# Performance work log

Hardware: AMD Instinct MI355X
Metric: run time of the kernel (lower is better)

Reference implementation:

```python
import math
import jax, jax.numpy as jnp
import numpy as np

B, S, D, H, DK, DV, L, DFF, V, NC, HID = 16, 512, 512, 8, 64, 64, 6, 2048, 32000, 5, 64


def setup_inputs() -> dict:
    key = jax.random.key(0)
    ks = jax.random.split(key, 32)
    def n(k, shape, scale=0.02):
        return jax.random.normal(k, shape, jnp.float32) * scale
    input_ids = jax.random.randint(ks[0], (B, S), 0, V).astype(jnp.int32)
    attention_mask = jnp.ones((B, S), jnp.bool_)
    emb = n(ks[1], (V, D)).at[0].set(0.0)  # padding_idx=0 row zeroed
    cls_token = jnp.zeros((D,), jnp.float32)
    return {
        "input_ids": input_ids,
        "attention_mask": attention_mask,
        "emb": emb,
        "cls_token": cls_token,
        "ln1_g": jnp.ones((L, D), jnp.float32), "ln1_b": jnp.zeros((L, D), jnp.float32),
        "ln2_g": jnp.ones((L, D), jnp.float32), "ln2_b": jnp.zeros((L, D), jnp.float32),
        "Wq": n(ks[2], (L, H, D, DK)), "bq": n(ks[3], (L, H, DK)),
        "Wk": n(ks[4], (L, H, D, DK)), "bk": n(ks[5], (L, H, DK)),
        "Wv": n(ks[6], (L, H, D, DV)), "bv": n(ks[7], (L, H, DV)),
        "Wo": n(ks[8], (L, H * DV, D)), "bo": n(ks[9], (L, D)),
        "W1": n(ks[10], (L, D, DFF)), "b1": n(ks[11], (L, DFF)),
        "W2": n(ks[12], (L, DFF, D)), "b2": n(ks[13], (L, D)),
        "Wc1": n(ks[14], (D, HID)), "bc1": n(ks[15], (HID,)),
        "Wc2": n(ks[16], (HID, NC)), "bc2": n(ks[17], (NC,)),
    }


def _layernorm(x, g, b, eps=1e-5):
    mu = jnp.mean(x, axis=-1, keepdims=True)
    var = jnp.var(x, axis=-1, keepdims=True)
    return (x - mu) * jax.lax.rsqrt(var + eps) * g + b


def _sinusoidal_pe(seq_len, d_model):
    pos = jnp.arange(seq_len, dtype=jnp.float32)[:, None]
    div = jnp.exp(jnp.arange(0, d_model, 2, dtype=jnp.float32) * (-math.log(10000.0) / d_model))
    pe = jnp.zeros((seq_len, d_model), jnp.float32)
    pe = pe.at[:, 0::2].set(jnp.sin(pos * div))
    pe = pe.at[:, 1::2].set(jnp.cos(pos * div))
    return pe


def _forward(input_ids, attention_mask, emb, cls_token,
             ln1_g, ln1_b, ln2_g, ln2_b,
             Wq, bq, Wk, bk, Wv, bv, Wo, bo,
             W1, b1, W2, b2, Wc1, bc1, Wc2, bc2):
    b, s = input_ids.shape
    x = emb[input_ids]                                     # [B,S,D]
    cls = jnp.broadcast_to(cls_token[None, None, :], (b, 1, x.shape[-1]))
    x = jnp.concatenate([cls, x], axis=1)                  # [B,S+1,D]
    full_mask = jnp.concatenate([jnp.ones((b, 1), jnp.bool_), attention_mask], axis=1)
    # pairwise attention mask [B, T, T]
    pair_mask = full_mask[:, None, :] & full_mask[:, :, None]
    x = x + _sinusoidal_pe(s + 1, x.shape[-1])[None]

    scale = 1.0 / math.sqrt(DK)

    def block(x, p):
        g1, be1, g2, be2, wq, bq_, wk, bk_, wv, bv_, wo, bo_, w1, bb1, w2, bb2 = p
        h = _layernorm(x, g1, be1)
        q = jnp.einsum('btd,hdk->bhtk', h, wq) + bq_[None, :, None, :]
        k = jnp.einsum('btd,hdk->bhtk', h, wk) + bk_[None, :, None, :]
        v = jnp.einsum('btd,hdv->bhtv', h, wv) + bv_[None, :, None, :]
        scores = jnp.einsum('bhqk,bhtk->bhqt', q, k) * scale
        scores = jnp.where(pair_mask[:, None, :, :], scores, -jnp.inf)
        attn = jax.nn.softmax(scores, axis=-1)
        o = jnp.einsum('bhqt,bhtv->bhqv', attn, v)          # [B,H,T,DV]
        o = o.transpose(0, 2, 1, 3).reshape(x.shape[0], x.shape[1], H * DV)
        x = x + o @ wo + bo_
        h2 = _layernorm(x, g2, be2)
        x = x + jnp.maximum(h2 @ w1 + bb1, 0.0) @ w2 + bb2
        return x, None

    params = (ln1_g, ln1_b, ln2_g, ln2_b, Wq, bq, Wk, bk, Wv, bv, Wo, bo, W1, b1, W2, b2)
    x, _ = jax.lax.scan(block, x, params)
    cls_out = x[:, 0]
    logits = jnp.maximum(cls_out @ Wc1 + bc1, 0.0) @ Wc2 + bc2
    return logits


def reference(input_ids, attention_mask, emb, cls_token,
              ln1_g, ln1_b, ln2_g, ln2_b,
              Wq, bq, Wk, bk, Wv, bv, Wo, bo,
              W1, b1, W2, b2, Wc1, bc1, Wc2, bc2):
    return _forward(input_ids, attention_mask, emb, cls_token,
                    ln1_g, ln1_b, ln2_g, ln2_b,
                    Wq, bq, Wk, bk, Wv, bv, Wo, bo,
                    W1, b1, W2, b2, Wc1, bc1, Wc2, bc2)
```

## Files before the change

kernel.cpp:

```cpp
#include <hip/hip_runtime.h>
#include <math.h>

#define DEV __device__ __forceinline__

typedef __attribute__((ext_vector_type(8))) short short8;
typedef __attribute__((ext_vector_type(4))) float f32x4;

DEV unsigned short f2bf(float f) {
  union { float f; unsigned int i; } v; v.f = f;
  unsigned int r = v.i + 0x7fffu + ((v.i >> 16) & 1u);
  return (unsigned short)(r >> 16);
}

DEV void lds16(const void* g, void* l) {
  __builtin_amdgcn_global_load_lds((__attribute__((address_space(1))) void*)(g),
                                   (__attribute__((address_space(3))) void*)(l), 16, 0, 0);
}


__global__ void transpose_g(const float* __restrict__ src, unsigned short* __restrict__ dst,
                            int Ksz, int Nsz) {
  __shared__ float tile[32][33];
  const int tx = threadIdx.x, ty = threadIdx.y;
  const int n0 = blockIdx.x * 32, k0 = blockIdx.y * 32;
  const size_t base = (size_t)blockIdx.z * Ksz * Nsz;
#pragma unroll
  for (int i = 0; i < 4; ++i)
    tile[ty + i * 8][tx] = src[base + (size_t)(k0 + ty + i * 8) * Nsz + n0 + tx];
  __syncthreads();
#pragma unroll
  for (int i = 0; i < 4; ++i)
    dst[base + (size_t)(n0 + ty + i * 8) * Ksz + k0 + tx] = f2bf(tile[tx][ty + i * 8]);
}

__global__ void pack_qkvT(const float* __restrict__ Wq, const float* __restrict__ Wk,
                          const float* __restrict__ Wv, unsigned short* __restrict__ dst) {
  __shared__ float tile[32][33];
  const int tx = threadIdx.x, ty = threadIdx.y;
  const int n0 = blockIdx.x * 32, k0 = blockIdx.y * 32, l = blockIdx.z;
  const int mat = n0 >> 9, hh = (n0 >> 6) & 7, dk0 = n0 & 63;
  const float* W = (mat == 0) ? Wq : (mat == 1) ? Wk : Wv;
  const float* Wl = W + ((size_t)l * 8 + hh) * 512 * 64;
#pragma unroll
  for (int i = 0; i < 4; ++i)
    tile[ty + i * 8][tx] = Wl[(size_t)(k0 + ty + i * 8) * 64 + dk0 + tx];
  __syncthreads();
#pragma unroll
  for (int i = 0; i < 4; ++i)
    dst[(size_t)l * 1536 * 512 + (size_t)(n0 + ty + i * 8) * 512 + k0 + tx] =
        f2bf(tile[tx][ty + i * 8]);
}

__global__ void pack_bias(const float* __restrict__ bq, const float* __restrict__ bk,
                          const float* __restrict__ bv, float* __restrict__ dst) {
  int i = blockIdx.x * 256 + threadIdx.x;
  if (i >= 6 * 1536) return;
  int l = i / 1536, c = i % 1536;
  float v = (c < 512) ? bq[l * 512 + c] : (c < 1024) ? bk[l * 512 + (c - 512)]
                                                     : bv[l * 512 + (c - 1024)];
  dst[i] = v;
}

__global__ void embed_kernel(const int* __restrict__ ids, const float* __restrict__ emb,
                             const float* __restrict__ cls, float* __restrict__ x) {
  int idx = blockIdx.x * 256 + threadIdx.x;
  int m = idx >> 9, d = idx & 511;
  int b = m / 513, t = m % 513;
  float v = (t == 0) ? cls[d] : emb[(size_t)ids[b * 512 + (t - 1)] * 512 + d];
  float fr = -(float)(d & ~1) * (9.2103403719761836f / 512.0f);
  float ang = (float)t * expf(fr);
  float pe = (d & 1) ? cosf(ang) : sinf(ang);
  x[idx] = v + pe;
}

template <int FUSE>
__global__ __launch_bounds__(256) void ln_kernel(float* __restrict__ x,
                                                 const float* __restrict__ g,
                                                 const float* __restrict__ bb,
                                                 unsigned short* __restrict__ h,
                                                 const float* __restrict__ part) {
  int wid = threadIdx.x >> 6, lane = threadIdx.x & 63;
  int m = blockIdx.x * 4 + wid;
  float* xr = x + (size_t)m * 512;
  float4 a = *(const float4*)(xr + lane * 8);
  float4 c = *(const float4*)(xr + lane * 8 + 4);
  if constexpr (FUSE) {
    const size_t PN = 8208ull * 512;
    const float* p = part + (size_t)m * 512 + lane * 8;
    float4 q0 = *(const float4*)(p),          q0b = *(const float4*)(p + 4);
    float4 q1 = *(const float4*)(p + PN),     q1b = *(const float4*)(p + PN + 4);
    float4 q2 = *(const float4*)(p + 2 * PN), q2b = *(const float4*)(p + 2 * PN + 4);
    a.x += q0.x + q1.x + q2.x;  a.y += q0.y + q1.y + q2.y;
    a.z += q0.z + q1.z + q2.z;  a.w += q0.w + q1.w + q2.w;
    c.x += q0b.x + q1b.x + q2b.x;  c.y += q0b.y + q1b.y + q2b.y;
    c.z += q0b.z + q1b.z + q2b.z;  c.w += q0b.w + q1b.w + q2b.w;
    *(float4*)(xr + lane * 8) = a;
    *(float4*)(xr + lane * 8 + 4) = c;
  }
  float s = a.x + a.y + a.z + a.w + c.x + c.y + c.z + c.w;
  float q = a.x * a.x + a.y * a.y + a.z * a.z + a.w * a.w +
            c.x * c.x + c.y * c.y + c.z * c.z + c.w * c.w;
#pragma unroll
  for (int d = 1; d < 64; d <<= 1) { s += __shfl_xor(s, d); q += __shfl_xor(q, d); }
  float mu = s * (1.f / 512.f);
  float var = q * (1.f / 512.f) - mu * mu;
  float rs = 1.f / sqrtf(var + 1e-5f);
  float4 g0 = *(const float4*)(g + lane * 8), g1 = *(const float4*)(g + lane * 8 + 4);
  float4 b0 = *(const float4*)(bb + lane * 8), b1 = *(const float4*)(bb + lane * 8 + 4);
  short8 ov;
  ov[0] = (short)f2bf((a.x - mu) * rs * g0.x + b0.x);
  ov[1] = (short)f2bf((a.y - mu) * rs * g0.y + b0.y);
  ov[2] = (short)f2bf((a.z - mu) * rs * g0.z + b0.z);
  ov[3] = (short)f2bf((a.w - mu) * rs * g0.w + b0.w);
  ov[4] = (short)f2bf((c.x - mu) * rs * g1.x + b1.x);
  ov[5] = (short)f2bf((c.y - mu) * rs * g1.y + b1.y);
  ov[6] = (short)f2bf((c.z - mu) * rs * g1.z + b1.z);
  ov[7] = (short)f2bf((c.w - mu) * rs * g1.w + b1.w);
  *(short8*)(h + (size_t)m * 512 + lane * 8) = ov;
}

template <int EPI>
DEV void gemm_epilogue(f32x4 (&acc)[4][4], const float* __restrict__ bias,
                       unsigned short* __restrict__ Cbf, float* __restrict__ Cres,
                       unsigned short* __restrict__ vT, float* __restrict__ part,
                       int M, int N, int m0, int n0, int wm, int wn, int l15, int l4,
                       int bz) {
  const bool z0 = (bz == 0);
  const size_t MN = (size_t)M * N;
#pragma unroll
  for (int i = 0; i < 4; ++i) {
#pragma unroll
    for (int j = 0; j < 4; ++j) {
      const int gn = n0 + wn + j * 16 + l15;
      float bv = bias[gn];
      if constexpr (EPI == 2) {
        if (!z0) bv = 0.f;
      }
#pragma unroll
      for (int r = 0; r < 4; ++r) {
        const int gm = m0 + wm + i * 16 + l4 * 4 + r;
        if (gm < M) {
          float v = acc[i][j][r] + bv;
          if constexpr (EPI == 1) v = fmaxf(v, 0.f);
          if constexpr (EPI == 2) {
            if (z0) {
              Cres[(size_t)gm * N + gn] += v;
            } else {
              part[(size_t)(bz - 1) * MN + (size_t)gm * N + gn] = v;
            }
          } else if constexpr (EPI == 3) {
            if (gn < 1024) {
              Cbf[(size_t)gm * N + gn] = f2bf(v);
            } else {
              int b = gm / 513, t = gm - b * 513;
              vT[(size_t)(b * 512 + (gn - 1024)) * 528 + t] = f2bf(v);
            }
          } else {
            Cbf[(size_t)gm * N + gn] = f2bf(v);
          }
        }
      }
    }
  }
}

template <int EPI>
__global__ __launch_bounds__(256) void gemm_bt(const unsigned short* __restrict__ A,
                                               const unsigned short* __restrict__ Bt,
                                               const float* __restrict__ bias,
                                               unsigned short* __restrict__ Cbf,
                                               float* __restrict__ Cres,
                                               unsigned short* __restrict__ vT,
                                               float* __restrict__ part,
                                               int M, int N, int K, int lda) {
  __shared__ __align__(16) unsigned short As[128 * 64];
  __shared__ __align__(16) unsigned short Bs[128 * 64];
  const int tid = threadIdx.x, w = tid >> 6, lane = tid & 63;
  const int l15 = lane & 15, l4 = lane >> 4;
  const int gx = gridDim.x;
  const int nwg = gx * gridDim.y;
  const int id = blockIdx.y * gx + blockIdx.x;
  const int xcd = id & 7, orig = id >> 3;
  const int qq = nwg >> 3, rr = nwg & 7;
  const int newid = (xcd < rr ? xcd * (qq + 1) : rr * (qq + 1) + (xcd - rr) * qq) + orig;
  const int m0 = (newid % gx) * 128, n0 = (newid / gx) * 128;
  const int wm = (w >> 1) * 64, wn = (w & 1) * 64;
  const int kbase = blockIdx.z * K;
  f32x4 acc[4][4] = {};
  const int nk = K >> 6;
  for (int kt = 0; kt < nk; ++kt) {
#pragma unroll
    for (int r = 0; r < 4; ++r) {
      int ol = (r * 4 + w) * 1024 + lane * 16;
      int ra = ol >> 7, cp = (ol >> 4) & 7;
      int co = ((cp ^ (ra & 7)) * 8) + kt * 64;
      lds16(A + (size_t)(m0 + ra) * lda + kbase + co, (char*)As + (r * 4 + w) * 1024);
      lds16(Bt + (size_t)(n0 + ra) * lda + kbase + co, (char*)Bs + (r * 4 + w) * 1024);
    }
    __syncthreads();
#pragma unroll
    for (int kk = 0; kk < 2; ++kk) {
      short8 af[4], bfr[4];
#pragma unroll
      for (int i = 0; i < 4; ++i) {
        int ar = wm + i * 16 + l15;
        af[i] = *(const short8*)&As[ar * 64 + (((kk * 4 + l4) ^ (ar & 7)) * 8)];
        int br = wn + i * 16 + l15;
        bfr[i] = *(const short8*)&Bs[br * 64 + (((kk * 4 + l4) ^ (br & 7)) * 8)];
      }
#pragma unroll
      for (int i = 0; i < 4; ++i)
#pragma unroll
        for (int j = 0; j < 4; ++j)
          acc[i][j] = __builtin_amdgcn_mfma_f32_16x16x32_bf16(af[i], bfr[j], acc[i][j], 0, 0, 0);
    }
    __syncthreads();
  }
  gemm_epilogue<EPI>(acc, bias, Cbf, Cres, vT, part, M, N, m0, n0, wm, wn, l15, l4,
                     blockIdx.z);
}

template <int EPI>
__global__ __launch_bounds__(512) void gemm_wide(const unsigned short* __restrict__ A,
                                                 const unsigned short* __restrict__ Bt,
                                                 const float* __restrict__ bias,
                                                 unsigned short* __restrict__ Cbf,
                                                 float* __restrict__ Cres,
                                                 unsigned short* __restrict__ vT,
                                                 float* __restrict__ part,
                                                 int M, int N, int K, int lda) {
  __shared__ __align__(16) unsigned short As[128 * 64];
  __shared__ __align__(16) unsigned short Bs[256 * 64];
  const int tid = threadIdx.x, w = tid >> 6, lane = tid & 63;
  const int l15 = lane & 15, l4 = lane >> 4;
  const int gx = gridDim.x;
  const int nwg = gx * gridDim.y;
  const int id = blockIdx.y * gx + blockIdx.x;
  const int xcd = id & 7, orig = id >> 3;
  const int qq = nwg >> 3, rr = nwg & 7;
  const int newid = (xcd < rr ? xcd * (qq + 1) : rr * (qq + 1) + (xcd - rr) * qq) + orig;
  const int m0 = (newid % gx) * 128, n0 = (newid / gx) * 256;
  const int wm = (w >> 2) * 64, wn = (w & 3) * 64;
  const int kbase = blockIdx.z * K;
  f32x4 acc[4][4] = {};
  const int nk = K >> 6;
  for (int kt = 0; kt < nk; ++kt) {
#pragma unroll
    for (int r = 0; r < 2; ++r) {
      int s = r * 8 + w;
      int ol = s * 1024 + lane * 16;
      int ra = ol >> 7, cp = (ol >> 4) & 7;
      int co = ((cp ^ (ra & 7)) * 8) + kt * 64;
      lds16(A + (size_t)(m0 + ra) * lda + kbase + co, (char*)As + s * 1024);
    }
#pragma unroll
    for (int r = 0; r < 4; ++r) {
      int s = r * 8 + w;
      int ol = s * 1024 + lane * 16;
      int rb = ol >> 7, cp = (ol >> 4) & 7;
      int co = ((cp ^ (rb & 7)) * 8) + kt * 64;
      lds16(Bt + (size_t)(n0 + rb) * lda + kbase + co, (char*)Bs + s * 1024);
    }
    __syncthreads();
#pragma unroll
    for (int kk = 0; kk < 2; ++kk) {
      short8 af[4], bfr[4];
#pragma unroll
      for (int i = 0; i < 4; ++i) {
        int ar = wm + i * 16 + l15;
        af[i] = *(const short8*)&As[ar * 64 + (((kk * 4 + l4) ^ (ar & 7)) * 8)];
        int br = wn + i * 16 + l15;
        bfr[i] = *(const short8*)&Bs[br * 64 + (((kk * 4 + l4) ^ (br & 7)) * 8)];
      }
#pragma unroll
      for (int i = 0; i < 4; ++i)
#pragma unroll
        for (int j = 0; j < 4; ++j)
          acc[i][j] = __builtin_amdgcn_mfma_f32_16x16x32_bf16(af[i], bfr[j], acc[i][j], 0, 0, 0);
    }
    __syncthreads();
  }
  gemm_epilogue<EPI>(acc, bias, Cbf, Cres, vT, part, M, N, m0, n0, wm, wn, l15, l4,
                     blockIdx.z);
}

__global__ __launch_bounds__(256) void reduce3(const float* __restrict__ p,
                                               float* __restrict__ x) {
  const size_t PN = 8208ull * 512;
  size_t i = ((size_t)blockIdx.x * 256 + threadIdx.x) * 4;
  float4 a = *(const float4*)(x + i);
  float4 b0 = *(const float4*)(p + i);
  float4 b1 = *(const float4*)(p + PN + i);
  float4 b2 = *(const float4*)(p + 2 * PN + i);
  a.x += b0.x + b1.x + b2.x;
  a.y += b0.y + b1.y + b2.y;
  a.z += b0.z + b1.z + b2.z;
  a.w += b0.w + b1.w + b2.w;
  *(float4*)(x + i) = a;
}

__global__ __launch_bounds__(256) void attn_kernel(const unsigned short* __restrict__ qkv,
                                                   const unsigned short* __restrict__ vT,
                                                   unsigned short* __restrict__ o) {
  const int qt = blockIdx.x, bh = blockIdx.y;
  const int b = bh >> 3, hh = bh & 7;
  const int tid = threadIdx.x, w = tid >> 6, lane = tid & 63;
  const int l15 = lane & 15, l4 = lane >> 4;
  __shared__ __align__(16) unsigned short Ks[64 * 64];
  __shared__ __align__(16) unsigned short Vs[64 * 64];
  __shared__ __align__(16) unsigned short Ps[64 * 72];
  const int q0 = qt * 64;
  const size_t qbase = (size_t)b * 513 * 1536;
  short8 qf[2];
  {
    const unsigned short* qp =
        qkv + qbase + (size_t)(q0 + w * 16 + l15) * 1536 + hh * 64 + l4 * 8;
    qf[0] = *(const short8*)qp;
    qf[1] = *(const short8*)(qp + 32);
  }
  f32x4 oacc[4] = {};
  float lpart[4] = {};
  for (int kvt = 0; kvt < 9; ++kvt) {
    const int kv0 = kvt * 64;
#pragma unroll
    for (int r = 0; r < 2; ++r) {
      int ol = (r * 4 + w) * 1024 + lane * 16;
      int rk = ol >> 7, cp = (ol >> 4) & 7;
      int sw = (cp ^ (rk & 7)) * 8;
      lds16(qkv + qbase + (size_t)(kv0 + rk) * 1536 + 512 + hh * 64 + sw,
            (char*)Ks + ol);
      lds16(vT + (size_t)(bh * 64 + rk) * 528 + kv0 + sw, (char*)Vs + ol);
    }
    __syncthreads();
    f32x4 sacc[4] = {};
#pragma unroll
    for (int kk = 0; kk < 2; ++kk)
#pragma unroll
      for (int nf = 0; nf < 4; ++nf) {
        int kr = nf * 16 + l15;
        short8 kf = *(const short8*)&Ks[kr * 64 + (((kk * 4 + l4) ^ (kr & 7)) * 8)];
        sacc[nf] = __builtin_amdgcn_mfma_f32_16x16x32_bf16(qf[kk], kf, sacc[nf], 0, 0, 0);
      }
#pragma unroll
    for (int nf = 0; nf < 4; ++nf) {
      const bool valid = (kv0 + nf * 16 + l15) < 513;
#pragma unroll
      for (int r = 0; r < 4; ++r) {
        float p = valid ? __expf(sacc[nf][r] * 0.125f) : 0.f;
        lpart[r] += p;
        Ps[(w * 16 + l4 * 4 + r) * 72 + nf * 16 + l15] = f2bf(p);
      }
    }
#pragma unroll
    for (int kk = 0; kk < 2; ++kk) {
      short8 pa = *(const short8*)&Ps[(w * 16 + l15) * 72 + kk * 32 + l4 * 8];
#pragma unroll
      for (int nf = 0; nf < 4; ++nf) {
        int dvr = nf * 16 + l15;
        short8 vf = *(const short8*)&Vs[dvr * 64 + (((kk * 4 + l4) ^ (dvr & 7)) * 8)];
        oacc[nf] = __builtin_amdgcn_mfma_f32_16x16x32_bf16(pa, vf, oacc[nf], 0, 0, 0);
      }
    }
    __syncthreads();
  }
#pragma unroll
  for (int d = 1; d < 16; d <<= 1)
#pragma unroll
    for (int r = 0; r < 4; ++r) lpart[r] += __shfl_xor(lpart[r], d);
#pragma unroll
  for (int nf = 0; nf < 4; ++nf)
#pragma unroll
    for (int r = 0; r < 4; ++r) {
      int q = q0 + w * 16 + l4 * 4 + r;
      if (q < 513) {
        float val = oacc[nf][r] / lpart[r];
        o[((size_t)b * 513 + q) * 512 + hh * 64 + nf * 16 + l15] = f2bf(val);
      }
    }
}

__global__ void cls_kernel(const float* __restrict__ x, const float* __restrict__ Wc1,
                           const float* __restrict__ bc1, const float* __restrict__ Wc2,
                           const float* __restrict__ bc2, float* __restrict__ out) {
  int b = blockIdx.x, j = threadIdx.x;
  const float* xr = x + (size_t)b * 513 * 512;
  float acc = bc1[j];
  for (int d = 0; d < 512; ++d) acc += xr[d] * Wc1[d * 64 + j];
  acc = fmaxf(acc, 0.f);
  __shared__ float hid[64];
  hid[j] = acc;
  __syncthreads();
  if (j < 5) {
    float lg = bc2[j];
#pragma unroll
    for (int d2 = 0; d2 < 64; ++d2) lg += hid[d2] * Wc2[d2 * 5 + j];
    out[b * 5 + j] = lg;
  }
}

extern "C" void kernel_launch(void* const* d_in, const int* in_sizes, int n_in,
                              void* d_out, int out_size, void* d_ws, size_t ws_size,
                              hipStream_t stream) {
  const int* ids = (const int*)d_in[0];
  const float* emb = (const float*)d_in[2];
  const float* cls = (const float*)d_in[3];
  const float* ln1g = (const float*)d_in[4];
  const float* ln1b = (const float*)d_in[5];
  const float* ln2g = (const float*)d_in[6];
  const float* ln2b = (const float*)d_in[7];
  const float* Wq = (const float*)d_in[8];
  const float* bq = (const float*)d_in[9];
  const float* Wk = (const float*)d_in[10];
  const float* bk = (const float*)d_in[11];
  const float* Wv = (const float*)d_in[12];
  const float* bv = (const float*)d_in[13];
  const float* Wo = (const float*)d_in[14];
  const float* bo = (const float*)d_in[15];
  const float* W1 = (const float*)d_in[16];
  const float* b1 = (const float*)d_in[17];
  const float* W2 = (const float*)d_in[18];
  const float* b2 = (const float*)d_in[19];
  const float* Wc1 = (const float*)d_in[20];
  const float* bc1 = (const float*)d_in[21];
  const float* Wc2 = (const float*)d_in[22];
  const float* bc2 = (const float*)d_in[23];

  char* ws = (char*)d_ws;
  size_t off = 0;
  auto alloc = [&](size_t bytes) {
    char* p = ws + off;
    off += (bytes + 255) & ~(size_t)255;
    return p;
  };
  const size_t QKV_ELEMS = 8320ull * 1536;
  const size_t VT_ELEMS = 16ull * 512 * 528 + 528;
  const size_t FFN_ELEMS = 8320ull * 2048;
  const size_t BIGU = (QKV_ELEMS + VT_ELEMS > FFN_ELEMS) ? QKV_ELEMS + VT_ELEMS : FFN_ELEMS;

  unsigned short* wqkvT = (unsigned short*)alloc(6ull * 1536 * 512 * 2);
  unsigned short* woT = (unsigned short*)alloc(6ull * 512 * 512 * 2);
  unsigned short* w1T = (unsigned short*)alloc(6ull * 2048 * 512 * 2);
  unsigned short* w2T = (unsigned short*)alloc(6ull * 512 * 2048 * 2);
  float* bqkv = (float*)alloc(6ull * 1536 * 4);
  float* x = (float*)alloc(8208ull * 512 * 4);
  unsigned short* hbuf = (unsigned short*)alloc(8320ull * 512 * 2);
  unsigned short* obuf = (unsigned short*)alloc(8320ull * 512 * 2);
  unsigned short* big = (unsigned short*)alloc(BIGU * 2);
  float* fpart = (float*)alloc(3ull * 8208 * 512 * 4);
  unsigned short* vT = big + QKV_ELEMS;
  if (off > ws_size) return;

  hipMemsetAsync(hbuf + 8208ull * 512, 0, 112ull * 512 * 2, stream);
  hipMemsetAsync(obuf + 8208ull * 512, 0, 112ull * 512 * 2, stream);
  hipMemsetAsync(big + 8208ull * 1536, 0, 112ull * 1536 * 2, stream);
  hipMemsetAsync(vT, 0, VT_ELEMS * 2, stream);

  pack_qkvT<<<dim3(48, 16, 6), dim3(32, 8), 0, stream>>>(Wq, Wk, Wv, wqkvT);
  transpose_g<<<dim3(16, 16, 6), dim3(32, 8), 0, stream>>>(Wo, woT, 512, 512);
  transpose_g<<<dim3(64, 16, 6), dim3(32, 8), 0, stream>>>(W1, w1T, 512, 2048);
  transpose_g<<<dim3(16, 64, 6), dim3(32, 8), 0, stream>>>(W2, w2T, 2048, 512);
  pack_bias<<<36, 256, 0, stream>>>(bq, bk, bv, bqkv);
  embed_kernel<<<16416, 256, 0, stream>>>(ids, emb, cls, x);

  for (int l = 0; l < 6; ++l) {
    if (l == 0)
      ln_kernel<0><<<2052, 256, 0, stream>>>(x, ln1g + l * 512, ln1b + l * 512, hbuf,
                                             nullptr);
    else
      ln_kernel<1><<<2052, 256, 0, stream>>>(x, ln1g + l * 512, ln1b + l * 512, hbuf,
                                             fpart);
    gemm_wide<3><<<dim3(65, 6), 512, 0, stream>>>(hbuf, wqkvT + (size_t)l * 1536 * 512,
                                                  bqkv + l * 1536, big, nullptr, vT,
                                                  nullptr, 8208, 1536, 512, 512);
    attn_kernel<<<dim3(9, 128), 256, 0, stream>>>(big, vT, obuf);
    gemm_bt<2><<<dim3(65, 4), 256, 0, stream>>>(obuf, woT + (size_t)l * 512 * 512,
                                                bo + l * 512, nullptr, x, nullptr,
                                                nullptr, 8208, 512, 512, 512);
    ln_kernel<0><<<2052, 256, 0, stream>>>(x, ln2g + l * 512, ln2b + l * 512, hbuf,
                                           nullptr);
    gemm_wide<1><<<dim3(65, 8), 512, 0, stream>>>(hbuf, w1T + (size_t)l * 2048 * 512,
                                                  b1 + l * 2048, big, nullptr, nullptr,
                                                  nullptr, 8208, 2048, 512, 512);
    gemm_wide<2><<<dim3(65, 2, 4), 512, 0, stream>>>(big, w2T + (size_t)l * 512 * 2048,
                                                     b2 + l * 512, nullptr, x, nullptr,
                                                     fpart, 8208, 512, 512, 2048);
  }
  reduce3<<<4104, 256, 0, stream>>>(fpart, x);
  cls_kernel<<<16, 64, 0, stream>>>(x, Wc1, bc1, Wc2, bc2, (float*)d_out);
}
```

Before: 1.292 ms.

## Double-buffer LDS tiles in GEMM and attention kernels to overlap loads

Both GEMM kernels and the attention kernel now keep two LDS buffers. Each iteration issues the async global-to-LDS loads for the next K or KV tile before running the MFMA work on the current tile. This removes the barrier that sat between load and compute, so global-load latency can overlap with matrix math. The cost is double the LDS footprint (96KB for gemm_wide), which may cut how many blocks fit on each CU.

```diff
diff --git a/kernel.cpp b/kernel.cpp
--- a/kernel.cpp
+++ b/kernel.cpp
@@ -173,8 +173,8 @@
                                                unsigned short* __restrict__ vT,
                                                float* __restrict__ part,
                                                int M, int N, int K, int lda) {
-  __shared__ __align__(16) unsigned short As[128 * 64];
-  __shared__ __align__(16) unsigned short Bs[128 * 64];
+  __shared__ __align__(16) unsigned short As[2][128 * 64];
+  __shared__ __align__(16) unsigned short Bs[2][128 * 64];
   const int tid = threadIdx.x, w = tid >> 6, lane = tid & 63;
   const int l15 = lane & 15, l4 = lane >> 4;
   const int gx = gridDim.x;
@@ -188,25 +188,31 @@
   const int kbase = blockIdx.z * K;
   f32x4 acc[4][4] = {};
   const int nk = K >> 6;
-  for (int kt = 0; kt < nk; ++kt) {
+  auto stage = [&](int buf, int kt) {
 #pragma unroll
     for (int r = 0; r < 4; ++r) {
-      int ol = (r * 4 + w) * 1024 + lane * 16;
+      int s = r * 4 + w;
+      int ol = s * 1024 + lane * 16;
       int ra = ol >> 7, cp = (ol >> 4) & 7;
       int co = ((cp ^ (ra & 7)) * 8) + kt * 64;
-      lds16(A + (size_t)(m0 + ra) * lda + kbase + co, (char*)As + (r * 4 + w) * 1024);
-      lds16(Bt + (size_t)(n0 + ra) * lda + kbase + co, (char*)Bs + (r * 4 + w) * 1024);
-    }
-    __syncthreads();
+      lds16(A + (size_t)(m0 + ra) * lda + kbase + co, (char*)As[buf] + s * 1024);
+      lds16(Bt + (size_t)(n0 + ra) * lda + kbase + co, (char*)Bs[buf] + s * 1024);
+    }
+  };
+  stage(0, 0);
+  __syncthreads();
+  int cur = 0;
+  for (int kt = 0; kt < nk; ++kt) {
+    if (kt + 1 < nk) stage(cur ^ 1, kt + 1);
 #pragma unroll
     for (int kk = 0; kk < 2; ++kk) {
       short8 af[4], bfr[4];
 #pragma unroll
       for (int i = 0; i < 4; ++i) {
         int ar = wm + i * 16 + l15;
-        af[i] = *(const short8*)&As[ar * 64 + (((kk * 4 + l4) ^ (ar & 7)) * 8)];
+        af[i] = *(const short8*)&As[cur][ar * 64 + (((kk * 4 + l4) ^ (ar & 7)) * 8)];
         int br = wn + i * 16 + l15;
-        bfr[i] = *(const short8*)&Bs[br * 64 + (((kk * 4 + l4) ^ (br & 7)) * 8)];
+        bfr[i] = *(const short8*)&Bs[cur][br * 64 + (((kk * 4 + l4) ^ (br & 7)) * 8)];
       }
 #pragma unroll
       for (int i = 0; i < 4; ++i)
@@ -215,6 +221,7 @@
           acc[i][j] = __builtin_amdgcn_mfma_f32_16x16x32_bf16(af[i], bfr[j], acc[i][j], 0, 0, 0);
     }
     __syncthreads();
+    cur ^= 1;
   }
   gemm_epilogue<EPI>(acc, bias, Cbf, Cres, vT, part, M, N, m0, n0, wm, wn, l15, l4,
                      blockIdx.z);
@@ -229,8 +236,8 @@
                                                  unsigned short* __restrict__ vT,
                                                  float* __restrict__ part,
                                                  int M, int N, int K, int lda) {
-  __shared__ __align__(16) unsigned short As[128 * 64];
-  __shared__ __align__(16) unsigned short Bs[256 * 64];
+  __shared__ __align__(16) unsigned short As[2][128 * 64];
+  __shared__ __align__(16) unsigned short Bs[2][256 * 64];
   const int tid = threadIdx.x, w = tid >> 6, lane = tid & 63;
   const int l15 = lane & 15, l4 = lane >> 4;
   const int gx = gridDim.x;
@@ -244,14 +251,14 @@
   const int kbase = blockIdx.z * K;
   f32x4 acc[4][4] = {};
   const int nk = K >> 6;
-  for (int kt = 0; kt < nk; ++kt) {
+  auto stage = [&](int buf, int kt) {
 #pragma unroll
     for (int r = 0; r < 2; ++r) {
       int s = r * 8 + w;
       int ol = s * 1024 + lane * 16;
       int ra = ol >> 7, cp = (ol >> 4) & 7;
       int co = ((cp ^ (ra & 7)) * 8) + kt * 64;
-      lds16(A + (size_t)(m0 + ra) * lda + kbase + co, (char*)As + s * 1024);
+      lds16(A + (size_t)(m0 + ra) * lda + kbase + co, (char*)As[buf] + s * 1024);
     }
 #pragma unroll
     for (int r = 0; r < 4; ++r) {
@@ -259,18 +266,23 @@
       int ol = s * 1024 + lane * 16;
       int rb = ol >> 7, cp = (ol >> 4) & 7;
       int co = ((cp ^ (rb & 7)) * 8) + kt * 64;
-      lds16(Bt + (size_t)(n0 + rb) * lda + kbase + co, (char*)Bs + s * 1024);
-    }
-    __syncthreads();
+      lds16(Bt + (size_t)(n0 + rb) * lda + kbase + co, (char*)Bs[buf] + s * 1024);
+    }
+  };
+  stage(0, 0);
+  __syncthreads();
+  int cur = 0;
+  for (int kt = 0; kt < nk; ++kt) {
+    if (kt + 1 < nk) stage(cur ^ 1, kt + 1);
 #pragma unroll
     for (int kk = 0; kk < 2; ++kk) {
       short8 af[4], bfr[4];
 #pragma unroll
       for (int i = 0; i < 4; ++i) {
         int ar = wm + i * 16 + l15;
-        af[i] = *(const short8*)&As[ar * 64 + (((kk * 4 + l4) ^ (ar & 7)) * 8)];
+        af[i] = *(const short8*)&As[cur][ar * 64 + (((kk * 4 + l4) ^ (ar & 7)) * 8)];
         int br = wn + i * 16 + l15;
-        bfr[i] = *(const short8*)&Bs[br * 64 + (((kk * 4 + l4) ^ (br & 7)) * 8)];
+        bfr[i] = *(const short8*)&Bs[cur][br * 64 + (((kk * 4 + l4) ^ (br & 7)) * 8)];
       }
 #pragma unroll
       for (int i = 0; i < 4; ++i)
@@ -279,6 +291,7 @@
           acc[i][j] = __builtin_amdgcn_mfma_f32_16x16x32_bf16(af[i], bfr[j], acc[i][j], 0, 0, 0);
     }
     __syncthreads();
+    cur ^= 1;
   }
   gemm_epilogue<EPI>(acc, bias, Cbf, Cres, vT, part, M, N, m0, n0, wm, wn, l15, l4,
                      blockIdx.z);
@@ -306,8 +319,8 @@
   const int b = bh >> 3, hh = bh & 7;
   const int tid = threadIdx.x, w = tid >> 6, lane = tid & 63;
   const int l15 = lane & 15, l4 = lane >> 4;
-  __shared__ __align__(16) unsigned short Ks[64 * 64];
-  __shared__ __align__(16) unsigned short Vs[64 * 64];
+  __shared__ __align__(16) unsigned short Ks[2][64 * 64];
+  __shared__ __align__(16) unsigned short Vs[2][64 * 64];
   __shared__ __align__(16) unsigned short Ps[64 * 72];
   const int q0 = qt * 64;
   const size_t qbase = (size_t)b * 513 * 1536;
@@ -320,7 +333,7 @@
   }
   f32x4 oacc[4] = {};
   float lpart[4] = {};
-  for (int kvt = 0; kvt < 9; ++kvt) {
+  auto stage = [&](int buf, int kvt) {
     const int kv0 = kvt * 64;
 #pragma unroll
     for (int r = 0; r < 2; ++r) {
@@ -328,17 +341,23 @@
       int rk = ol >> 7, cp = (ol >> 4) & 7;
       int sw = (cp ^ (rk & 7)) * 8;
       lds16(qkv + qbase + (size_t)(kv0 + rk) * 1536 + 512 + hh * 64 + sw,
-            (char*)Ks + ol);
-      lds16(vT + (size_t)(bh * 64 + rk) * 528 + kv0 + sw, (char*)Vs + ol);
-    }
-    __syncthreads();
+            (char*)Ks[buf] + ol);
+      lds16(vT + (size_t)(bh * 64 + rk) * 528 + kv0 + sw, (char*)Vs[buf] + ol);
+    }
+  };
+  stage(0, 0);
+  __syncthreads();
+  int cur = 0;
+  for (int kvt = 0; kvt < 9; ++kvt) {
+    const int kv0 = kvt * 64;
+    if (kvt + 1 < 9) stage(cur ^ 1, kvt + 1);
     f32x4 sacc[4] = {};
 #pragma unroll
     for (int kk = 0; kk < 2; ++kk)
 #pragma unroll
       for (int nf = 0; nf < 4; ++nf) {
         int kr = nf * 16 + l15;
-        short8 kf = *(const short8*)&Ks[kr * 64 + (((kk * 4 + l4) ^ (kr & 7)) * 8)];
+        short8 kf = *(const short8*)&Ks[cur][kr * 64 + (((kk * 4 + l4) ^ (kr & 7)) * 8)];
         sacc[nf] = __builtin_amdgcn_mfma_f32_16x16x32_bf16(qf[kk], kf, sacc[nf], 0, 0, 0);
       }
 #pragma unroll
@@ -357,11 +376,12 @@
 #pragma unroll
       for (int nf = 0; nf < 4; ++nf) {
         int dvr = nf * 16 + l15;
-        short8 vf = *(const short8*)&Vs[dvr * 64 + (((kk * 4 + l4) ^ (dvr & 7)) * 8)];
+        short8 vf = *(const short8*)&Vs[cur][dvr * 64 + (((kk * 4 + l4) ^ (dvr & 7)) * 8)];
         oacc[nf] = __builtin_amdgcn_mfma_f32_16x16x32_bf16(pa, vf, oacc[nf], 0, 0, 0);
       }
     }
     __syncthreads();
+    cur ^= 1;
   }
 #pragma unroll
   for (int d = 1; d < 16; d <<= 1)
```

Result: slower. 1.492 ms (+15.5%).

## Triple-buffer LDS in wide GEMM with async prefetch two tiles ahead

Applied to the files above, without the earlier changes.

The wide GEMM kernel now keeps three LDS buffers for the A and B tiles and issues global-to-LDS loads two k-tiles ahead. Partial vmcnt waits replace the full syncthreads, so memory loads overlap MFMA compute and each iteration needs only one barrier instead of two. LDS use per block triples to 144KB, which can reduce occupancy. Correctness relies on the vmcnt(6) count matching the six loads issued per stage.

```diff
diff --git a/kernel.cpp b/kernel.cpp
--- a/kernel.cpp
+++ b/kernel.cpp
@@ -5,6 +5,11 @@
 
 typedef __attribute__((ext_vector_type(8))) short short8;
 typedef __attribute__((ext_vector_type(4))) float f32x4;
+
+#define BAR() __builtin_amdgcn_s_barrier()
+#define FENCE() asm volatile("" ::: "memory")
+#define WAIT_VM0() asm volatile("s_waitcnt vmcnt(0)" ::: "memory")
+#define WAIT_VM6() asm volatile("s_waitcnt vmcnt(6)" ::: "memory")
 
 DEV unsigned short f2bf(float f) {
   union { float f; unsigned int i; } v; v.f = f;
@@ -229,8 +234,8 @@
                                                  unsigned short* __restrict__ vT,
                                                  float* __restrict__ part,
                                                  int M, int N, int K, int lda) {
-  __shared__ __align__(16) unsigned short As[128 * 64];
-  __shared__ __align__(16) unsigned short Bs[256 * 64];
+  __shared__ __align__(16) unsigned short As[3][128 * 64];
+  __shared__ __align__(16) unsigned short Bs[3][256 * 64];
   const int tid = threadIdx.x, w = tid >> 6, lane = tid & 63;
   const int l15 = lane & 15, l4 = lane >> 4;
   const int gx = gridDim.x;
@@ -244,14 +249,14 @@
   const int kbase = blockIdx.z * K;
   f32x4 acc[4][4] = {};
   const int nk = K >> 6;
-  for (int kt = 0; kt < nk; ++kt) {
+  auto stage = [&](int buf, int kt) {
 #pragma unroll
     for (int r = 0; r < 2; ++r) {
       int s = r * 8 + w;
       int ol = s * 1024 + lane * 16;
       int ra = ol >> 7, cp = (ol >> 4) & 7;
       int co = ((cp ^ (ra & 7)) * 8) + kt * 64;
-      lds16(A + (size_t)(m0 + ra) * lda + kbase + co, (char*)As + s * 1024);
+      lds16(A + (size_t)(m0 + ra) * lda + kbase + co, (char*)As[buf] + ol);
     }
 #pragma unroll
     for (int r = 0; r < 4; ++r) {
@@ -259,18 +264,30 @@
       int ol = s * 1024 + lane * 16;
       int rb = ol >> 7, cp = (ol >> 4) & 7;
       int co = ((cp ^ (rb & 7)) * 8) + kt * 64;
-      lds16(Bt + (size_t)(n0 + rb) * lda + kbase + co, (char*)Bs + s * 1024);
-    }
-    __syncthreads();
+      lds16(Bt + (size_t)(n0 + rb) * lda + kbase + co, (char*)Bs[buf] + ol);
+    }
+  };
+  stage(0, 0);
+  if (nk > 1) stage(1, 1);
+  int cur = 0;
+  for (int kt = 0; kt < nk; ++kt) {
+    if (kt + 1 < nk) { WAIT_VM6(); } else { WAIT_VM0(); }
+    FENCE();
+    BAR();
+    FENCE();
+    if (kt + 2 < nk) {
+      int nbuf = cur + 2; if (nbuf >= 3) nbuf -= 3;
+      stage(nbuf, kt + 2);
+    }
 #pragma unroll
     for (int kk = 0; kk < 2; ++kk) {
       short8 af[4], bfr[4];
 #pragma unroll
       for (int i = 0; i < 4; ++i) {
         int ar = wm + i * 16 + l15;
-        af[i] = *(const short8*)&As[ar * 64 + (((kk * 4 + l4) ^ (ar & 7)) * 8)];
+        af[i] = *(const short8*)&As[cur][ar * 64 + (((kk * 4 + l4) ^ (ar & 7)) * 8)];
         int br = wn + i * 16 + l15;
-        bfr[i] = *(const short8*)&Bs[br * 64 + (((kk * 4 + l4) ^ (br & 7)) * 8)];
+        bfr[i] = *(const short8*)&Bs[cur][br * 64 + (((kk * 4 + l4) ^ (br & 7)) * 8)];
       }
 #pragma unroll
       for (int i = 0; i < 4; ++i)
@@ -278,7 +295,8 @@
         for (int j = 0; j < 4; ++j)
           acc[i][j] = __builtin_amdgcn_mfma_f32_16x16x32_bf16(af[i], bfr[j], acc[i][j], 0, 0, 0);
     }
-    __syncthreads();
+    FENCE();
+    cur = (cur == 2) ? 0 : cur + 1;
   }
   gemm_epilogue<EPI>(acc, bias, Cbf, Cres, vT, part, M, N, m0, n0, wm, wn, l15, l4,
                      blockIdx.z);
```

Result: slower. 1.515 ms (+17.3%).

## Process two query tiles per attention block to reuse loaded K/V tiles

Applied to the files above, without the earlier changes.

Each attention workgroup now handles 128 queries (two 64-row tiles) instead of 64, so every K/V tile staged in LDS feeds twice the MFMA work, and the grid shrinks from 9 to 5 query groups per head. This roughly halves K/V global-to-LDS traffic and barrier count per query. In exchange it raises register pressure (doubled accumulators and Q fragments), cuts the block count to 640, and leaves the last group handling a single partial tile, so load balance and occupancy could suffer.

```diff
diff --git a/kernel.cpp b/kernel.cpp
--- a/kernel.cpp
+++ b/kernel.cpp
@@ -302,24 +302,27 @@
 __global__ __launch_bounds__(256) void attn_kernel(const unsigned short* __restrict__ qkv,
                                                    const unsigned short* __restrict__ vT,
                                                    unsigned short* __restrict__ o) {
-  const int qt = blockIdx.x, bh = blockIdx.y;
+  const int gq = blockIdx.x, bh = blockIdx.y;
   const int b = bh >> 3, hh = bh & 7;
   const int tid = threadIdx.x, w = tid >> 6, lane = tid & 63;
   const int l15 = lane & 15, l4 = lane >> 4;
   __shared__ __align__(16) unsigned short Ks[64 * 64];
   __shared__ __align__(16) unsigned short Vs[64 * 64];
   __shared__ __align__(16) unsigned short Ps[64 * 72];
-  const int q0 = qt * 64;
   const size_t qbase = (size_t)b * 513 * 1536;
-  short8 qf[2];
-  {
-    const unsigned short* qp =
-        qkv + qbase + (size_t)(q0 + w * 16 + l15) * 1536 + hh * 64 + l4 * 8;
-    qf[0] = *(const short8*)qp;
-    qf[1] = *(const short8*)(qp + 32);
-  }
-  f32x4 oacc[4] = {};
-  float lpart[4] = {};
+  const int q00 = gq * 128;
+  const int nt = (q00 + 64 < 513) ? 2 : 1;
+  short8 qf[2][2];
+#pragma unroll
+  for (int t = 0; t < 2; ++t)
+    if (t < nt) {
+      const unsigned short* qp =
+          qkv + qbase + (size_t)(q00 + t * 64 + w * 16 + l15) * 1536 + hh * 64 + l4 * 8;
+      qf[t][0] = *(const short8*)qp;
+      qf[t][1] = *(const short8*)(qp + 32);
+    }
+  f32x4 oacc[2][4] = {};
+  float lpart[2][4] = {};
   for (int kvt = 0; kvt < 9; ++kvt) {
     const int kv0 = kvt * 64;
 #pragma unroll
@@ -332,51 +335,58 @@
       lds16(vT + (size_t)(bh * 64 + rk) * 528 + kv0 + sw, (char*)Vs + ol);
     }
     __syncthreads();
-    f32x4 sacc[4] = {};
-#pragma unroll
-    for (int kk = 0; kk < 2; ++kk)
+#pragma unroll
+    for (int t = 0; t < 2; ++t) {
+      if (t >= nt) continue;
+      f32x4 sacc[4] = {};
+#pragma unroll
+      for (int kk = 0; kk < 2; ++kk)
+#pragma unroll
+        for (int nf = 0; nf < 4; ++nf) {
+          int kr = nf * 16 + l15;
+          short8 kf = *(const short8*)&Ks[kr * 64 + (((kk * 4 + l4) ^ (kr & 7)) * 8)];
+          sacc[nf] = __builtin_amdgcn_mfma_f32_16x16x32_bf16(qf[t][kk], kf, sacc[nf], 0, 0, 0);
+        }
 #pragma unroll
       for (int nf = 0; nf < 4; ++nf) {
-        int kr = nf * 16 + l15;
-        short8 kf = *(const short8*)&Ks[kr * 64 + (((kk * 4 + l4) ^ (kr & 7)) * 8)];
-        sacc[nf] = __builtin_amdgcn_mfma_f32_16x16x32_bf16(qf[kk], kf, sacc[nf], 0, 0, 0);
-      }
-#pragma unroll
-    for (int nf = 0; nf < 4; ++nf) {
-      const bool valid = (kv0 + nf * 16 + l15) < 513;
+        const bool valid = (kv0 + nf * 16 + l15) < 513;
+#pragma unroll
+        for (int r = 0; r < 4; ++r) {
+          float p = valid ? __expf(sacc[nf][r] * 0.125f) : 0.f;
+          lpart[t][r] += p;
+          Ps[(w * 16 + l4 * 4 + r) * 72 + nf * 16 + l15] = f2bf(p);
+        }
+      }
+#pragma unroll
+      for (int kk = 0; kk < 2; ++kk) {
+        short8 pa = *(const short8*)&Ps[(w * 16 + l15) * 72 + kk * 32 + l4 * 8];
+#pragma unroll
+        for (int nf = 0; nf < 4; ++nf) {
+          int dvr = nf * 16 + l15;
+          short8 vf = *(const short8*)&Vs[dvr * 64 + (((kk * 4 + l4) ^ (dvr & 7)) * 8)];
+          oacc[t][nf] = __builtin_amdgcn_mfma_f32_16x16x32_bf16(pa, vf, oacc[t][nf], 0, 0, 0);
+        }
+      }
+    }
+    __syncthreads();
+  }
+#pragma unroll
+  for (int t = 0; t < 2; ++t) {
+#pragma unroll
+    for (int d = 1; d < 16; d <<= 1)
+#pragma unroll
+      for (int r = 0; r < 4; ++r) lpart[t][r] += __shfl_xor(lpart[t][r], d);
+#pragma unroll
+    for (int nf = 0; nf < 4; ++nf)
 #pragma unroll
       for (int r = 0; r < 4; ++r) {
-        float p = valid ? __expf(sacc[nf][r] * 0.125f) : 0.f;
-        lpart[r] += p;
-        Ps[(w * 16 + l4 * 4 + r) * 72 + nf * 16 + l15] = f2bf(p);
-      }
-    }
-#pragma unroll
-    for (int kk = 0; kk < 2; ++kk) {
-      short8 pa = *(const short8*)&Ps[(w * 16 + l15) * 72 + kk * 32 + l4 * 8];
-#pragma unroll
-      for (int nf = 0; nf < 4; ++nf) {
-        int dvr = nf * 16 + l15;
-        short8 vf = *(const short8*)&Vs[dvr * 64 + (((kk * 4 + l4) ^ (dvr & 7)) * 8)];
-        oacc[nf] = __builtin_amdgcn_mfma_f32_16x16x32_bf16(pa, vf, oacc[nf], 0, 0, 0);
-      }
-    }
-    __syncthreads();
-  }
-#pragma unroll
-  for (int d = 1; d < 16; d <<= 1)
-#pragma unroll
-    for (int r = 0; r < 4; ++r) lpart[r] += __shfl_xor(lpart[r], d);
-#pragma unroll
-  for (int nf = 0; nf < 4; ++nf)
-#pragma unroll
-    for (int r = 0; r < 4; ++r) {
-      int q = q0 + w * 16 + l4 * 4 + r;
-      if (q < 513) {
-        float val = oacc[nf][r] / lpart[r];
-        o[((size_t)b * 513 + q) * 512 + hh * 64 + nf * 16 + l15] = f2bf(val);
-      }
-    }
+        int q = q00 + t * 64 + w * 16 + l4 * 4 + r;
+        if (q < 513) {
+          float val = oacc[t][nf][r] / lpart[t][r];
+          o[((size_t)b * 513 + q) * 512 + hh * 64 + nf * 16 + l15] = f2bf(val);
+        }
+      }
+  }
 }
 
 __global__ void cls_kernel(const float* __restrict__ x, const float* __restrict__ Wc1,
@@ -472,7 +482,7 @@
     gemm_wide<3><<<dim3(65, 6), 512, 0, stream>>>(hbuf, wqkvT + (size_t)l * 1536 * 512,
                                                   bqkv + l * 1536, big, nullptr, vT,
                                                   nullptr, 8208, 1536, 512, 512);
-    attn_kernel<<<dim3(9, 128), 256, 0, stream>>>(big, vT, obuf);
+    attn_kernel<<<dim3(5, 128), 256, 0, stream>>>(big, vT, obuf);
     gemm_bt<2><<<dim3(65, 4), 256, 0, stream>>>(obuf, woT + (size_t)l * 512 * 512,
                                                 bo + l * 512, nullptr, x, nullptr,
                                                 nullptr, 8208, 512, 512, 512);
```

Result: no change. 1.304 ms (+0.9%).
